# Kernel optimization log

Measured on AMD Instinct MI355X. Metric: run time of the kernel, lower is better.

The kernel has to match this reference:

```python
import jax, jax.numpy as jnp
import numpy as np

K = 9  # 3x3 kernel taps

def _conv3x3(x, w, b):
    # standard 3x3 conv, stride 1, pad 1, NCHW
    y = jax.lax.conv_general_dilated(x, w, (1, 1), [(1, 1), (1, 1)],
                                     dimension_numbers=('NCHW', 'OIHW', 'NCHW'))
    return y + b[None, :, None, None]

def setup_inputs() -> dict:
    key = jax.random.key(0)
    ks = jax.random.split(key, 4)
    B, C, Cout, H, W = 2, 256, 256, 128, 128
    x = jax.random.normal(ks[0], (B, C, H, W), jnp.float32)
    w_off = jax.random.normal(ks[1], (3 * K, C, 3, 3), jnp.float32) * 0.01
    b_off = jnp.zeros((3 * K,), jnp.float32)
    weight = jax.random.normal(ks[2], (Cout, C, 3, 3), jnp.float32) * (1.0 / np.sqrt(K * C))
    bias = jnp.zeros((Cout,), jnp.float32)
    gamma = jnp.ones((Cout,), jnp.float32)
    beta = jnp.zeros((Cout,), jnp.float32)
    return {"x": x, "w_off": w_off, "b_off": b_off, "weight": weight,
            "bias": bias, "gamma": gamma, "beta": beta}

def _deform_gather(x, off_y, off_x, mask):
    # x: [B,C,H,W]; off_y/off_x/mask: [B,K,H,W]
    # returns modulated bilinear samples [B,C,K,H,W]
    B, C, H, W = x.shape
    kh = (jnp.arange(K, dtype=x.dtype) // 3).reshape(1, K, 1, 1)
    kw = (jnp.arange(K, dtype=x.dtype) % 3).reshape(1, K, 1, 1)
    # sampling position per tap: base - pad + tap*dilation + learned offset
    py = jnp.arange(H, dtype=x.dtype).reshape(1, 1, H, 1) - 1.0 + kh + off_y
    px = jnp.arange(W, dtype=x.dtype).reshape(1, 1, 1, W) - 1.0 + kw + off_x
    y0 = jnp.floor(py); x0 = jnp.floor(px)
    wy1 = py - y0; wx1 = px - x0
    xf = x.reshape(B, C, H * W)
    def corner(iy, ix, wgt):
        valid = (iy >= 0) & (iy <= H - 1) & (ix >= 0) & (ix <= W - 1)
        iyc = jnp.clip(iy, 0, H - 1).astype(jnp.int32)
        ixc = jnp.clip(ix, 0, W - 1).astype(jnp.int32)
        lin = (iyc * W + ixc).reshape(B, 1, K * H * W)
        g = jnp.take_along_axis(xf, lin, axis=2).reshape(B, C, K, H, W)
        return g * jnp.where(valid, wgt, 0.0)[:, None]  # zero outside borders
    val = (corner(y0,     x0,     (1 - wy1) * (1 - wx1))
         + corner(y0,     x0 + 1, (1 - wy1) * wx1)
         + corner(y0 + 1, x0,     wy1 * (1 - wx1))
         + corner(y0 + 1, x0 + 1, wy1 * wx1))
    return val * mask[:, None]

def reference(x, w_off, b_off, weight, bias, gamma, beta):
    B, C, H, W = x.shape
    om = _conv3x3(x, w_off, b_off)  # [B, 3K, H, W]
    off_y = om[:, :K]
    off_x = om[:, K:2 * K]
    m = jax.nn.sigmoid(om[:, 2 * K:])  # modulation mask
    sampled = _deform_gather(x, off_y, off_x, m)  # [B,C,K,H,W]
    Cout = weight.shape[0]
    y = jnp.einsum('bckhw,ock->bohw', sampled, weight.reshape(Cout, C, K))
    y = y + bias[None, :, None, None]
    # BatchNorm2d (training-mode batch stats, eps=1e-5) + ReLU
    mu = jnp.mean(y, axis=(0, 2, 3), keepdims=True)
    var = jnp.var(y, axis=(0, 2, 3), keepdims=True)
    yn = (y - mu) * jax.lax.rsqrt(var + 1e-5)
    return jax.nn.relu(yn * gamma[None, :, None, None] + beta[None, :, None, None])
```

## Files before the change

### kernel.cpp

```cpp
#include <hip/hip_runtime.h>
#include <math.h>

#define HW 16384
#define Cc 256
#define CO 256

typedef unsigned short u16;
typedef unsigned int   u32;
typedef __attribute__((ext_vector_type(8))) short bf16x8;
typedef __attribute__((ext_vector_type(4))) float f32x4;

__device__ __forceinline__ u16 f2bf(float f) {
    u32 u = __float_as_uint(f);
    u32 r = (u + 0x7fffu + ((u >> 16) & 1u)) >> 16;
    return (u16)r;
}
__device__ __forceinline__ float bl(u32 u) { return __uint_as_float(u << 16); }
__device__ __forceinline__ float bh(u32 u) { return __uint_as_float(u & 0xffff0000u); }
__device__ __forceinline__ u32 pkbf(float lo, float hi) {
    u32 ul = __float_as_uint(lo), uh = __float_as_uint(hi);
    u32 rl = (ul + 0x7fffu + ((ul >> 16) & 1u)) >> 16;
    u32 rh = (uh + 0x7fffu + ((uh >> 16) & 1u)) & 0xffff0000u;
    return rl | rh;
}

__global__ void k_prep(const float* __restrict__ w, const float* __restrict__ wof,
                       const float* __restrict__ bof,
                       u16* __restrict__ wfr, u16* __restrict__ wofr,
                       float* __restrict__ om) {
    int id = blockIdx.x * 256 + threadIdx.x;
    if (id < 589824) {
        int i    = id & 7;
        int lane = (id >> 3) & 63;
        int fb   = id >> 9;
        int k32  = fb % 72;
        int ot   = fb / 72;
        int o  = ot * 16 + (lane & 15);
        int K  = k32 * 32 + (lane >> 4) * 8 + i;
        int kt = K >> 8;
        int c  = K & 255;
        wfr[id] = f2bf(w[((size_t)o * 256 + c) * 9 + kt]);
    } else if (id < 663552) {
        int id2  = id - 589824;
        int i    = id2 & 7;
        int lane = (id2 >> 3) & 63;
        int fb   = id2 >> 9;
        int k32  = fb % 72;
        int mt   = fb / 72;
        int o  = mt * 16 + (lane & 15);
        int K  = k32 * 32 + (lane >> 4) * 8 + i;
        int t  = K >> 8;
        int c  = K & 255;
        float v = (o < 27) ? wof[((size_t)o * 256 + c) * 9 + t] : 0.0f;
        wofr[id2] = f2bf(v);
    } else {
        int id3 = id - 663552;
        om[id3] = bof[(id3 >> 14) % 27];
    }
}

__global__ __launch_bounds__(256) void k_xt(const float* __restrict__ x, u16* __restrict__ Xt) {
    const int tid = threadIdx.x;
    const int bid = blockIdx.x;
    const int hw0 = (bid & 255) * 64;
    const int b   = bid >> 8;
    const int hwl = tid & 63;
    const int cg  = tid >> 6;
    const int hw  = hw0 + hwl;
    const float* xb = x + ((size_t)b << 22);
    u16* dst = Xt + (((size_t)b << 14) + hw) * 256 + cg * 64;
    #pragma unroll
    for (int oct = 0; oct < 8; ++oct) {
        int c0 = cg * 64 + oct * 8;
        u32 pk[4];
        #pragma unroll
        for (int q = 0; q < 4; ++q) {
            float v0 = xb[((size_t)(c0 + 2 * q) << 14) + hw];
            float v1 = xb[((size_t)(c0 + 2 * q + 1) << 14) + hw];
            pk[q] = (u32)f2bf(v0) | ((u32)f2bf(v1) << 16);
        }
        *(uint4*)(dst + oct * 8) = make_uint4(pk[0], pk[1], pk[2], pk[3]);
    }
}

__global__ __launch_bounds__(256) void k_offmfma(const u16* __restrict__ Xt,
                                                 const u16* __restrict__ wofr,
                                                 float* __restrict__ om) {
    const int tid  = threadIdx.x;
    const int wid  = tid >> 6;
    const int lane = tid & 63;
    const int bid  = blockIdx.x;
    const int kq   = bid & 3;
    const int wq   = (bid >> 2) & 1;
    const int h    = (bid >> 3) & 127;
    const int b    = bid >> 10;

    const int lr = lane & 15;
    const int lg = lane >> 4;
    const int w  = wq * 64 + wid * 16 + lr;

    f32x4 acc0 = (f32x4)0.0f, acc1 = (f32x4)0.0f;
    const u16* XtB = Xt + (((size_t)b << 14) << 8);

    #pragma unroll 3
    for (int k32 = kq * 18; k32 < kq * 18 + 18; ++k32) {
        int t   = k32 >> 3;
        int c32 = k32 & 7;
        int dh  = t / 3 - 1;
        int dw  = t % 3 - 1;
        int hh  = h + dh;
        int ww  = w + dw;
        bool valid = (hh >= 0) && (hh < 128) && (ww >= 0) && (ww < 128);
        int hc = min(max(hh, 0), 127);
        int wc = min(max(ww, 0), 127);
        bf16x8 bv = *(const bf16x8*)(XtB + ((size_t)(hc * 128 + wc) << 8) + c32 * 32 + lg * 8);
        if (!valid) bv = (bf16x8)0;
        bf16x8 a0 = *(const bf16x8*)(wofr + (((size_t)k32 * 64 + lane) << 3));
        bf16x8 a1 = *(const bf16x8*)(wofr + ((((size_t)(72 + k32)) * 64 + lane) << 3));
        acc0 = __builtin_amdgcn_mfma_f32_16x16x32_bf16(a0, bv, acc0, 0, 0, 0);
        acc1 = __builtin_amdgcn_mfma_f32_16x16x32_bf16(a1, bv, acc1, 0, 0, 0);
    }

    float* omb = om + ((size_t)b * 27 << 14) + h * 128 + w;
    #pragma unroll
    for (int j = 0; j < 4; ++j) {
        int o = lg * 4 + j;
        atomicAdd(omb + ((size_t)o << 14), acc0[j]);
        int o1 = 16 + lg * 4 + j;
        if (o1 < 27) atomicAdd(omb + ((size_t)o1 << 14), acc1[j]);
    }
}

__global__ __launch_bounds__(512) void k_sgemm(const u16* __restrict__ Xt,
                                               const float* __restrict__ om,
                                               const u16* __restrict__ wfr,
                                               const float* __restrict__ bias,
                                               float* __restrict__ y,
                                               float* __restrict__ psum) {
    __shared__ int4   soff[9][64];
    __shared__ float4 swt[9][64];
    __shared__ __align__(16) u16 Blds[2][4096];

    const int tid  = threadIdx.x;
    const int wid  = tid >> 6;
    const int lane = tid & 63;
    const int bid  = ((blockIdx.x & 7) << 6) | (blockIdx.x >> 3);
    const int p0   = bid * 64;
    const int b    = p0 >> 14;
    const int hwb  = p0 & 16383;

    for (int e = tid; e < 576; e += 512) {
        int t = e >> 6, j = e & 63;
        int hw = hwb + j;
        int h = hw >> 7, wc = hw & 127;
        const size_t ob = (size_t)b * 27 * HW;
        float oy = om[ob + (size_t)t * HW + hw];
        float ox = om[ob + (size_t)(9 + t) * HW + hw];
        float mv = om[ob + (size_t)(18 + t) * HW + hw];
        mv = 1.0f / (1.0f + expf(-mv));
        float py = (float)h - 1.0f + (float)(t / 3) + oy;
        float px = (float)wc - 1.0f + (float)(t % 3) + ox;
        float y0f = floorf(py), x0f = floorf(px);
        float wy = py - y0f, wx = px - x0f;
        int iy = (int)y0f, ix = (int)x0f;
        float w4[4] = {(1.0f - wy) * (1.0f - wx), (1.0f - wy) * wx,
                       wy * (1.0f - wx),          wy * wx};
        const int dy[4] = {0, 0, 1, 1};
        const int dx[4] = {0, 1, 0, 1};
        int of[4]; float cw[4];
        #pragma unroll
        for (int r = 0; r < 4; ++r) {
            int yy = iy + dy[r], xx = ix + dx[r];
            bool v = (yy >= 0) && (yy <= 127) && (xx >= 0) && (xx <= 127);
            int yc = min(max(yy, 0), 127);
            int xc = min(max(xx, 0), 127);
            of[r] = yc * 128 + xc;
            cw[r] = v ? w4[r] * mv : 0.0f;
        }
        soff[t][j] = make_int4(of[0], of[1], of[2], of[3]);
        swt[t][j]  = make_float4(cw[0], cw[1], cw[2], cw[3]);
    }
    __syncthreads();

    const int jp    = tid >> 3;
    const int kloc8 = (((tid & 7) ^ (jp & 7)) << 3);
    const u16* XtB  = Xt + (((size_t)b << 14) << 8);

    const int lg = lane >> 4;
    const int lr = lane & 15;

    f32x4 acc[2][4];
    #pragma unroll
    for (int m = 0; m < 2; ++m)
        #pragma unroll
        for (int n = 0; n < 4; ++n) acc[m][n] = (f32x4)0.0f;

    auto gload = [&](int s, uint4* gg) {
        int t = s >> 2;
        int c = ((s & 3) << 6) + kloc8;
        int4 oa = soff[t][jp];
        gg[0] = *(const uint4*)(XtB + (size_t)oa.x * 256 + c);
        gg[1] = *(const uint4*)(XtB + (size_t)oa.y * 256 + c);
        gg[2] = *(const uint4*)(XtB + (size_t)oa.z * 256 + c);
        gg[3] = *(const uint4*)(XtB + (size_t)oa.w * 256 + c);
    };
    auto gcomb = [&](int s, const uint4* gg, int buf) {
        int t = s >> 2;
        float4 ca = swt[t][jp];
        const u32* gw = (const u32*)gg;
        u32 o4[4];
        #pragma unroll
        for (int q = 0; q < 4; ++q) {
            float lo = ca.x * bl(gw[q])     + ca.y * bl(gw[4 + q])
                     + ca.z * bl(gw[8 + q]) + ca.w * bl(gw[12 + q]);
            float hi = ca.x * bh(gw[q])     + ca.y * bh(gw[4 + q])
                     + ca.z * bh(gw[8 + q]) + ca.w * bh(gw[12 + q]);
            o4[q] = pkbf(lo, hi);
        }
        *(uint4*)((char*)&Blds[buf][0] + tid * 16) = make_uint4(o4[0], o4[1], o4[2], o4[3]);
    };
    auto aload = [&](int k32g, bf16x8 dst2[2][2]) {
        #pragma unroll
        for (int kk = 0; kk < 2; ++kk)
            #pragma unroll
            for (int m = 0; m < 2; ++m)
                dst2[kk][m] = *(const bf16x8*)(wfr +
                    ((size_t)((wid * 2 + m) * 72 + k32g + kk) << 9) + (size_t)lane * 8);
    };

    bf16x8 af[2][2];
    {
        uint4 g[4];
        gload(0, g);
        aload(0, af);
        gcomb(0, g, 0);
    }
    __syncthreads();

    int cur = 0;
    for (int s = 0; s < 36; ++s) {
        const int nxt = cur ^ 1;
        uint4 gn[4];
        bf16x8 afn[2][2];
        if (s < 35) {
            gload(s + 1, gn);
            aload(2 * (s + 1), afn);
        }

        const char* bb2 = (const char*)&Blds[cur][0];
        #pragma unroll
        for (int kk = 0; kk < 2; ++kk) {
            bf16x8 bfv[4];
            #pragma unroll
            for (int n = 0; n < 4; ++n) {
                int row  = n * 16 + lr;
                int boff = row * 128 + ((kk * 64 + lg * 16) ^ ((row & 7) << 4));
                bfv[n] = *(const bf16x8*)(bb2 + boff);
            }
            #pragma unroll
            for (int m = 0; m < 2; ++m)
                #pragma unroll
                for (int n = 0; n < 4; ++n)
                    acc[m][n] = __builtin_amdgcn_mfma_f32_16x16x32_bf16(af[kk][m], bfv[n], acc[m][n], 0, 0, 0);
        }

        if (s < 35) {
            gcomb(s + 1, gn, nxt);
            #pragma unroll
            for (int kk = 0; kk < 2; ++kk)
                #pragma unroll
                for (int m = 0; m < 2; ++m)
                    af[kk][m] = afn[kk][m];
        }
        __syncthreads();
        cur = nxt;
    }

    const int hw0  = hwb + lr;
    const int slot = (bid & 31) << 9;
    #pragma unroll
    for (int m = 0; m < 2; ++m) {
        #pragma unroll
        for (int jj = 0; jj < 4; ++jj) {
            int o = wid * 32 + m * 16 + lg * 4 + jj;
            float bv = bias[o];
            float* ya = y + ((size_t)b * 256 + o) * HW + hw0;
            float ssum = 0.0f, ssq = 0.0f;
            #pragma unroll
            for (int n = 0; n < 4; ++n) {
                float v = acc[m][n][jj] + bv;
                ya[n * 16] = v;
                ssum += v;
                ssq  += v * v;
            }
            #pragma unroll
            for (int d = 1; d < 16; d <<= 1) {
                ssum += __shfl_xor(ssum, d);
                ssq  += __shfl_xor(ssq, d);
            }
            if (lr == 0) {
                atomicAdd(&psum[slot + o], ssum);
                atomicAdd(&psum[slot + 256 + o], ssq);
            }
        }
    }
}

__global__ void k_stats2(const float* __restrict__ psum, float* __restrict__ st) {
    int o = threadIdx.x;
    float s = 0.0f, q = 0.0f;
    #pragma unroll 8
    for (int r = 0; r < 32; ++r) {
        s += psum[(r << 9) + o];
        q += psum[(r << 9) + 256 + o];
    }
    float mu  = s / 32768.0f;
    float var = q / 32768.0f - mu * mu;
    st[o]       = mu;
    st[256 + o] = rsqrtf(var + 1e-5f);
}

__global__ void k_norm(const float* __restrict__ y, const float* __restrict__ stats,
                       const float* __restrict__ gamma, const float* __restrict__ beta,
                       float* __restrict__ out) {
    int i4 = blockIdx.x * 256 + threadIdx.x;
    if (i4 >= (2 * CO * HW) / 4) return;
    int o = (i4 >> 12) & 255;
    float g  = gamma[o] * stats[256 + o];
    float bt = beta[o] - stats[o] * g;
    float4 v = ((const float4*)y)[i4];
    float4 r;
    r.x = fmaxf(fmaf(v.x, g, bt), 0.0f);
    r.y = fmaxf(fmaf(v.y, g, bt), 0.0f);
    r.z = fmaxf(fmaf(v.z, g, bt), 0.0f);
    r.w = fmaxf(fmaf(v.w, g, bt), 0.0f);
    ((float4*)out)[i4] = r;
}

extern "C" void kernel_launch(void* const* d_in, const int* in_sizes, int n_in,
                              void* d_out, int out_size, void* d_ws, size_t ws_size,
                              hipStream_t stream) {
    const float* x      = (const float*)d_in[0];
    const float* w_off  = (const float*)d_in[1];
    const float* b_off  = (const float*)d_in[2];
    const float* weight = (const float*)d_in[3];
    const float* bias   = (const float*)d_in[4];
    const float* gamma  = (const float*)d_in[5];
    const float* beta   = (const float*)d_in[6];
    float* out = (float*)d_out;

    float* ws   = (float*)d_ws;
    float* om   = ws;
    float* st   = om + 884736;
    float* ps   = st + 512;
    float* yb   = ps + 16384;
    u16*   wfr  = (u16*)(yb + 8388608);
    u16*   wofr = wfr + 589824;
    u16*   Xt   = wofr + 73728;

    k_prep<<<6048, 256, 0, stream>>>(weight, w_off, b_off, wfr, wofr, om);
    k_xt<<<512, 256, 0, stream>>>(x, Xt);
    hipMemsetAsync(ps, 0, 16384 * sizeof(float), stream);
    k_offmfma<<<2048, 256, 0, stream>>>(Xt, wofr, om);

    k_sgemm<<<512, 512, 0, stream>>>(Xt, om, wfr, bias, yb, ps);

    k_stats2<<<1, 256, 0, stream>>>(ps, st);
    k_norm<<<(2 * CO * HW / 4 + 255) / 256, 256, 0, stream>>>(yb, st, gamma, beta, out);
}
```

Baseline: 134.1 us.

## Drop split-K atomics in offset conv and double-buffer gather loads in sgemm

```diff
diff --git a/kernel.cpp b/kernel.cpp
--- a/kernel.cpp
+++ b/kernel.cpp
@@ -25,9 +25,7 @@
 }
 
 __global__ void k_prep(const float* __restrict__ w, const float* __restrict__ wof,
-                       const float* __restrict__ bof,
-                       u16* __restrict__ wfr, u16* __restrict__ wofr,
-                       float* __restrict__ om) {
+                       u16* __restrict__ wfr, u16* __restrict__ wofr) {
     int id = blockIdx.x * 256 + threadIdx.x;
     if (id < 589824) {
         int i    = id & 7;
@@ -53,9 +51,6 @@
         int c  = K & 255;
         float v = (o < 27) ? wof[((size_t)o * 256 + c) * 9 + t] : 0.0f;
         wofr[id2] = f2bf(v);
-    } else {
-        int id3 = id - 663552;
-        om[id3] = bof[(id3 >> 14) % 27];
     }
 }
 
@@ -85,15 +80,15 @@
 
 __global__ __launch_bounds__(256) void k_offmfma(const u16* __restrict__ Xt,
                                                  const u16* __restrict__ wofr,
+                                                 const float* __restrict__ bof,
                                                  float* __restrict__ om) {
     const int tid  = threadIdx.x;
     const int wid  = tid >> 6;
     const int lane = tid & 63;
     const int bid  = blockIdx.x;
-    const int kq   = bid & 3;
-    const int wq   = (bid >> 2) & 1;
-    const int h    = (bid >> 3) & 127;
-    const int b    = bid >> 10;
+    const int wq   = bid & 1;
+    const int h    = (bid >> 1) & 127;
+    const int b    = bid >> 8;
 
     const int lr = lane & 15;
     const int lg = lane >> 4;
@@ -102,32 +97,34 @@
     f32x4 acc0 = (f32x4)0.0f, acc1 = (f32x4)0.0f;
     const u16* XtB = Xt + (((size_t)b << 14) << 8);
 
-    #pragma unroll 3
-    for (int k32 = kq * 18; k32 < kq * 18 + 18; ++k32) {
-        int t   = k32 >> 3;
-        int c32 = k32 & 7;
-        int dh  = t / 3 - 1;
-        int dw  = t % 3 - 1;
-        int hh  = h + dh;
-        int ww  = w + dw;
+    for (int t = 0; t < 9; ++t) {
+        int dh = t / 3 - 1;
+        int dw = t % 3 - 1;
+        int hh = h + dh;
+        int ww = w + dw;
         bool valid = (hh >= 0) && (hh < 128) && (ww >= 0) && (ww < 128);
         int hc = min(max(hh, 0), 127);
         int wc = min(max(ww, 0), 127);
-        bf16x8 bv = *(const bf16x8*)(XtB + ((size_t)(hc * 128 + wc) << 8) + c32 * 32 + lg * 8);
-        if (!valid) bv = (bf16x8)0;
-        bf16x8 a0 = *(const bf16x8*)(wofr + (((size_t)k32 * 64 + lane) << 3));
-        bf16x8 a1 = *(const bf16x8*)(wofr + ((((size_t)(72 + k32)) * 64 + lane) << 3));
-        acc0 = __builtin_amdgcn_mfma_f32_16x16x32_bf16(a0, bv, acc0, 0, 0, 0);
-        acc1 = __builtin_amdgcn_mfma_f32_16x16x32_bf16(a1, bv, acc1, 0, 0, 0);
+        const u16* xrow = XtB + ((size_t)(hc * 128 + wc) << 8) + lg * 8;
+        #pragma unroll
+        for (int c32 = 0; c32 < 8; ++c32) {
+            int k32 = t * 8 + c32;
+            bf16x8 bv = *(const bf16x8*)(xrow + c32 * 32);
+            if (!valid) bv = (bf16x8)0;
+            bf16x8 a0 = *(const bf16x8*)(wofr + (((size_t)k32 * 64 + lane) << 3));
+            bf16x8 a1 = *(const bf16x8*)(wofr + ((((size_t)(72 + k32)) * 64 + lane) << 3));
+            acc0 = __builtin_amdgcn_mfma_f32_16x16x32_bf16(a0, bv, acc0, 0, 0, 0);
+            acc1 = __builtin_amdgcn_mfma_f32_16x16x32_bf16(a1, bv, acc1, 0, 0, 0);
+        }
     }
 
     float* omb = om + ((size_t)b * 27 << 14) + h * 128 + w;
     #pragma unroll
     for (int j = 0; j < 4; ++j) {
         int o = lg * 4 + j;
-        atomicAdd(omb + ((size_t)o << 14), acc0[j]);
+        omb[(size_t)o << 14] = acc0[j] + bof[o];
         int o1 = 16 + lg * 4 + j;
-        if (o1 < 27) atomicAdd(omb + ((size_t)o1 << 14), acc1[j]);
+        if (o1 < 27) omb[(size_t)o1 << 14] = acc1[j] + bof[o1];
     }
 }
 
@@ -227,26 +224,7 @@
                 dst2[kk][m] = *(const bf16x8*)(wfr +
                     ((size_t)((wid * 2 + m) * 72 + k32g + kk) << 9) + (size_t)lane * 8);
     };
-
-    bf16x8 af[2][2];
-    {
-        uint4 g[4];
-        gload(0, g);
-        aload(0, af);
-        gcomb(0, g, 0);
-    }
-    __syncthreads();
-
-    int cur = 0;
-    for (int s = 0; s < 36; ++s) {
-        const int nxt = cur ^ 1;
-        uint4 gn[4];
-        bf16x8 afn[2][2];
-        if (s < 35) {
-            gload(s + 1, gn);
-            aload(2 * (s + 1), afn);
-        }
-
+    auto domfma = [&](int cur, bf16x8 afv[2][2]) {
         const char* bb2 = (const char*)&Blds[cur][0];
         #pragma unroll
         for (int kk = 0; kk < 2; ++kk) {
@@ -261,19 +239,47 @@
             for (int m = 0; m < 2; ++m)
                 #pragma unroll
                 for (int n = 0; n < 4; ++n)
-                    acc[m][n] = __builtin_amdgcn_mfma_f32_16x16x32_bf16(af[kk][m], bfv[n], acc[m][n], 0, 0, 0);
-        }
-
-        if (s < 35) {
-            gcomb(s + 1, gn, nxt);
+                    acc[m][n] = __builtin_amdgcn_mfma_f32_16x16x32_bf16(afv[kk][m], bfv[n], acc[m][n], 0, 0, 0);
+        }
+    };
+
+    bf16x8 af[2][2], afn[2][2];
+    uint4 gA[4], gB[4];
+    {
+        uint4 t0[4];
+        gload(0, t0);
+        aload(0, af);
+        gcomb(0, t0, 0);
+        gload(1, gA);
+    }
+    __syncthreads();
+
+    int cur = 0;
+    for (int sp = 0; sp < 18; ++sp) {
+        const int s0 = 2 * sp;
+        const int s1 = s0 + 1;
+        if (s0 < 34) gload(s0 + 2, gB);
+        aload(2 * (s0 + 1), afn);
+        domfma(cur, af);
+        gcomb(s0 + 1, gA, cur ^ 1);
+        #pragma unroll
+        for (int kk = 0; kk < 2; ++kk)
+            #pragma unroll
+            for (int m = 0; m < 2; ++m) af[kk][m] = afn[kk][m];
+        __syncthreads();
+        cur ^= 1;
+        if (s1 < 34) gload(s1 + 2, gA);
+        if (s1 < 35) aload(2 * (s1 + 1), afn);
+        domfma(cur, af);
+        if (s1 < 35) {
+            gcomb(s1 + 1, gB, cur ^ 1);
             #pragma unroll
             for (int kk = 0; kk < 2; ++kk)
                 #pragma unroll
-                for (int m = 0; m < 2; ++m)
-                    af[kk][m] = afn[kk][m];
+                for (int m = 0; m < 2; ++m) af[kk][m] = afn[kk][m];
         }
         __syncthreads();
-        cur = nxt;
+        cur ^= 1;
     }
 
     const int hw0  = hwb + lr;
@@ -358,10 +364,10 @@
     u16*   wofr = wfr + 589824;
     u16*   Xt   = wofr + 73728;
 
-    k_prep<<<6048, 256, 0, stream>>>(weight, w_off, b_off, wfr, wofr, om);
+    k_prep<<<2592, 256, 0, stream>>>(weight, w_off, wfr, wofr);
     k_xt<<<512, 256, 0, stream>>>(x, Xt);
     hipMemsetAsync(ps, 0, 16384 * sizeof(float), stream);
-    k_offmfma<<<2048, 256, 0, stream>>>(Xt, wofr, om);
+    k_offmfma<<<512, 256, 0, stream>>>(Xt, wofr, b_off, om);
 
     k_sgemm<<<512, 512, 0, stream>>>(Xt, om, wfr, bias, yb, ps);
 
```

Measured after the change: 136.5 us. No clear change (+1.8%).

## Switch to fp16 MFMA with packed half2 bilinear combine; drop split-K atomics

Applied to the files above, without the earlier changes.

```diff
diff --git a/kernel.cpp b/kernel.cpp
--- a/kernel.cpp
+++ b/kernel.cpp
@@ -1,4 +1,5 @@
 #include <hip/hip_runtime.h>
+#include <hip/hip_fp16.h>
 #include <math.h>
 
 #define HW 16384
@@ -7,27 +8,15 @@
 
 typedef unsigned short u16;
 typedef unsigned int   u32;
-typedef __attribute__((ext_vector_type(8))) short bf16x8;
+typedef __attribute__((ext_vector_type(8))) _Float16 f16x8;
 typedef __attribute__((ext_vector_type(4))) float f32x4;
 
-__device__ __forceinline__ u16 f2bf(float f) {
-    u32 u = __float_as_uint(f);
-    u32 r = (u + 0x7fffu + ((u >> 16) & 1u)) >> 16;
-    return (u16)r;
-}
-__device__ __forceinline__ float bl(u32 u) { return __uint_as_float(u << 16); }
-__device__ __forceinline__ float bh(u32 u) { return __uint_as_float(u & 0xffff0000u); }
-__device__ __forceinline__ u32 pkbf(float lo, float hi) {
-    u32 ul = __float_as_uint(lo), uh = __float_as_uint(hi);
-    u32 rl = (ul + 0x7fffu + ((ul >> 16) & 1u)) >> 16;
-    u32 rh = (uh + 0x7fffu + ((uh >> 16) & 1u)) & 0xffff0000u;
-    return rl | rh;
+__device__ __forceinline__ u16 f2h(float f) {
+    return __half_as_ushort(__float2half(f));
 }
 
 __global__ void k_prep(const float* __restrict__ w, const float* __restrict__ wof,
-                       const float* __restrict__ bof,
-                       u16* __restrict__ wfr, u16* __restrict__ wofr,
-                       float* __restrict__ om) {
+                       u16* __restrict__ wfr, u16* __restrict__ wofr) {
     int id = blockIdx.x * 256 + threadIdx.x;
     if (id < 589824) {
         int i    = id & 7;
@@ -39,7 +28,7 @@
         int K  = k32 * 32 + (lane >> 4) * 8 + i;
         int kt = K >> 8;
         int c  = K & 255;
-        wfr[id] = f2bf(w[((size_t)o * 256 + c) * 9 + kt]);
+        wfr[id] = f2h(w[((size_t)o * 256 + c) * 9 + kt]);
     } else if (id < 663552) {
         int id2  = id - 589824;
         int i    = id2 & 7;
@@ -52,10 +41,7 @@
         int t  = K >> 8;
         int c  = K & 255;
         float v = (o < 27) ? wof[((size_t)o * 256 + c) * 9 + t] : 0.0f;
-        wofr[id2] = f2bf(v);
-    } else {
-        int id3 = id - 663552;
-        om[id3] = bof[(id3 >> 14) % 27];
+        wofr[id2] = f2h(v);
     }
 }
 
@@ -77,7 +63,7 @@
         for (int q = 0; q < 4; ++q) {
             float v0 = xb[((size_t)(c0 + 2 * q) << 14) + hw];
             float v1 = xb[((size_t)(c0 + 2 * q + 1) << 14) + hw];
-            pk[q] = (u32)f2bf(v0) | ((u32)f2bf(v1) << 16);
+            pk[q] = (u32)f2h(v0) | ((u32)f2h(v1) << 16);
         }
         *(uint4*)(dst + oct * 8) = make_uint4(pk[0], pk[1], pk[2], pk[3]);
     }
@@ -85,15 +71,15 @@
 
 __global__ __launch_bounds__(256) void k_offmfma(const u16* __restrict__ Xt,
                                                  const u16* __restrict__ wofr,
+                                                 const float* __restrict__ bof,
                                                  float* __restrict__ om) {
     const int tid  = threadIdx.x;
     const int wid  = tid >> 6;
     const int lane = tid & 63;
     const int bid  = blockIdx.x;
-    const int kq   = bid & 3;
-    const int wq   = (bid >> 2) & 1;
-    const int h    = (bid >> 3) & 127;
-    const int b    = bid >> 10;
+    const int wq   = bid & 1;
+    const int h    = (bid >> 1) & 127;
+    const int b    = bid >> 8;
 
     const int lr = lane & 15;
     const int lg = lane >> 4;
@@ -102,32 +88,34 @@
     f32x4 acc0 = (f32x4)0.0f, acc1 = (f32x4)0.0f;
     const u16* XtB = Xt + (((size_t)b << 14) << 8);
 
-    #pragma unroll 3
-    for (int k32 = kq * 18; k32 < kq * 18 + 18; ++k32) {
-        int t   = k32 >> 3;
-        int c32 = k32 & 7;
-        int dh  = t / 3 - 1;
-        int dw  = t % 3 - 1;
-        int hh  = h + dh;
-        int ww  = w + dw;
+    for (int t = 0; t < 9; ++t) {
+        int dh = t / 3 - 1;
+        int dw = t % 3 - 1;
+        int hh = h + dh;
+        int ww = w + dw;
         bool valid = (hh >= 0) && (hh < 128) && (ww >= 0) && (ww < 128);
         int hc = min(max(hh, 0), 127);
         int wc = min(max(ww, 0), 127);
-        bf16x8 bv = *(const bf16x8*)(XtB + ((size_t)(hc * 128 + wc) << 8) + c32 * 32 + lg * 8);
-        if (!valid) bv = (bf16x8)0;
-        bf16x8 a0 = *(const bf16x8*)(wofr + (((size_t)k32 * 64 + lane) << 3));
-        bf16x8 a1 = *(const bf16x8*)(wofr + ((((size_t)(72 + k32)) * 64 + lane) << 3));
-        acc0 = __builtin_amdgcn_mfma_f32_16x16x32_bf16(a0, bv, acc0, 0, 0, 0);
-        acc1 = __builtin_amdgcn_mfma_f32_16x16x32_bf16(a1, bv, acc1, 0, 0, 0);
+        const u16* xrow = XtB + ((size_t)(hc * 128 + wc) << 8) + lg * 8;
+        #pragma unroll
+        for (int c32 = 0; c32 < 8; ++c32) {
+            int k32 = t * 8 + c32;
+            f16x8 bv = *(const f16x8*)(xrow + c32 * 32);
+            if (!valid) bv = (f16x8)0;
+            f16x8 a0 = *(const f16x8*)(wofr + (((size_t)k32 * 64 + lane) << 3));
+            f16x8 a1 = *(const f16x8*)(wofr + ((((size_t)(72 + k32)) * 64 + lane) << 3));
+            acc0 = __builtin_amdgcn_mfma_f32_16x16x32_f16(a0, bv, acc0, 0, 0, 0);
+            acc1 = __builtin_amdgcn_mfma_f32_16x16x32_f16(a1, bv, acc1, 0, 0, 0);
+        }
     }
 
     float* omb = om + ((size_t)b * 27 << 14) + h * 128 + w;
     #pragma unroll
     for (int j = 0; j < 4; ++j) {
         int o = lg * 4 + j;
-        atomicAdd(omb + ((size_t)o << 14), acc0[j]);
+        omb[(size_t)o << 14] = acc0[j] + bof[o];
         int o1 = 16 + lg * 4 + j;
-        if (o1 < 27) atomicAdd(omb + ((size_t)o1 << 14), acc1[j]);
+        if (o1 < 27) omb[(size_t)o1 << 14] = acc1[j] + bof[o1];
     }
 }
 
@@ -137,8 +125,8 @@
                                                const float* __restrict__ bias,
                                                float* __restrict__ y,
                                                float* __restrict__ psum) {
-    __shared__ int4   soff[9][64];
-    __shared__ float4 swt[9][64];
+    __shared__ int4    soff[9][64];
+    __shared__ __half2 swt2[9][64][4];
     __shared__ __align__(16) u16 Blds[2][4096];
 
     const int tid  = threadIdx.x;
@@ -167,7 +155,7 @@
                        wy * (1.0f - wx),          wy * wx};
         const int dy[4] = {0, 0, 1, 1};
         const int dx[4] = {0, 1, 0, 1};
-        int of[4]; float cw[4];
+        int of[4];
         #pragma unroll
         for (int r = 0; r < 4; ++r) {
             int yy = iy + dy[r], xx = ix + dx[r];
@@ -175,10 +163,9 @@
             int yc = min(max(yy, 0), 127);
             int xc = min(max(xx, 0), 127);
             of[r] = yc * 128 + xc;
-            cw[r] = v ? w4[r] * mv : 0.0f;
+            swt2[t][j][r] = __float2half2_rn(v ? w4[r] * mv : 0.0f);
         }
         soff[t][j] = make_int4(of[0], of[1], of[2], of[3]);
-        swt[t][j]  = make_float4(cw[0], cw[1], cw[2], cw[3]);
     }
     __syncthreads();
 
@@ -206,29 +193,35 @@
     };
     auto gcomb = [&](int s, const uint4* gg, int buf) {
         int t = s >> 2;
-        float4 ca = swt[t][jp];
-        const u32* gw = (const u32*)gg;
+        __half2 w0 = swt2[t][jp][0];
+        __half2 w1 = swt2[t][jp][1];
+        __half2 w2 = swt2[t][jp][2];
+        __half2 w3 = swt2[t][jp][3];
+        const __half2* c0 = (const __half2*)&gg[0];
+        const __half2* c1 = (const __half2*)&gg[1];
+        const __half2* c2 = (const __half2*)&gg[2];
+        const __half2* c3 = (const __half2*)&gg[3];
         u32 o4[4];
         #pragma unroll
         for (int q = 0; q < 4; ++q) {
-            float lo = ca.x * bl(gw[q])     + ca.y * bl(gw[4 + q])
-                     + ca.z * bl(gw[8 + q]) + ca.w * bl(gw[12 + q]);
-            float hi = ca.x * bh(gw[q])     + ca.y * bh(gw[4 + q])
-                     + ca.z * bh(gw[8 + q]) + ca.w * bh(gw[12 + q]);
-            o4[q] = pkbf(lo, hi);
+            __half2 o = __hmul2(c0[q], w0);
+            o = __hfma2(c1[q], w1, o);
+            o = __hfma2(c2[q], w2, o);
+            o = __hfma2(c3[q], w3, o);
+            o4[q] = *(const u32*)&o;
         }
         *(uint4*)((char*)&Blds[buf][0] + tid * 16) = make_uint4(o4[0], o4[1], o4[2], o4[3]);
     };
-    auto aload = [&](int k32g, bf16x8 dst2[2][2]) {
+    auto aload = [&](int k32g, f16x8 dst2[2][2]) {
         #pragma unroll
         for (int kk = 0; kk < 2; ++kk)
             #pragma unroll
             for (int m = 0; m < 2; ++m)
-                dst2[kk][m] = *(const bf16x8*)(wfr +
+                dst2[kk][m] = *(const f16x8*)(wfr +
                     ((size_t)((wid * 2 + m) * 72 + k32g + kk) << 9) + (size_t)lane * 8);
     };
 
-    bf16x8 af[2][2];
+    f16x8 af[2][2];
     {
         uint4 g[4];
         gload(0, g);
@@ -241,7 +234,7 @@
     for (int s = 0; s < 36; ++s) {
         const int nxt = cur ^ 1;
         uint4 gn[4];
-        bf16x8 afn[2][2];
+        f16x8 afn[2][2];
         if (s < 35) {
             gload(s + 1, gn);
             aload(2 * (s + 1), afn);
@@ -250,18 +243,18 @@
         const char* bb2 = (const char*)&Blds[cur][0];
         #pragma unroll
         for (int kk = 0; kk < 2; ++kk) {
-            bf16x8 bfv[4];
+            f16x8 bfv[4];
             #pragma unroll
             for (int n = 0; n < 4; ++n) {
                 int row  = n * 16 + lr;
                 int boff = row * 128 + ((kk * 64 + lg * 16) ^ ((row & 7) << 4));
-                bfv[n] = *(const bf16x8*)(bb2 + boff);
+                bfv[n] = *(const f16x8*)(bb2 + boff);
             }
             #pragma unroll
             for (int m = 0; m < 2; ++m)
                 #pragma unroll
                 for (int n = 0; n < 4; ++n)
-                    acc[m][n] = __builtin_amdgcn_mfma_f32_16x16x32_bf16(af[kk][m], bfv[n], acc[m][n], 0, 0, 0);
+                    acc[m][n] = __builtin_amdgcn_mfma_f32_16x16x32_f16(af[kk][m], bfv[n], acc[m][n], 0, 0, 0);
         }
 
         if (s < 35) {
@@ -358,10 +351,10 @@
     u16*   wofr = wfr + 589824;
     u16*   Xt   = wofr + 73728;
 
-    k_prep<<<6048, 256, 0, stream>>>(weight, w_off, b_off, wfr, wofr, om);
+    k_prep<<<2592, 256, 0, stream>>>(weight, w_off, wfr, wofr);
     k_xt<<<512, 256, 0, stream>>>(x, Xt);
     hipMemsetAsync(ps, 0, 16384 * sizeof(float), stream);
-    k_offmfma<<<2048, 256, 0, stream>>>(Xt, wofr, om);
+    k_offmfma<<<512, 256, 0, stream>>>(Xt, wofr, b_off, om);
 
     k_sgemm<<<512, 512, 0, stream>>>(Xt, om, wfr, bias, yb, ps);
 
```

New measurement: 123.8 us. 1.08x faster.
